# Kernel optimization log

Hardware: AMD Instinct MI355X
Metric: run time of the kernel (lower is better)

Reference implementation:

```python
import math
import jax, jax.numpy as jnp
import numpy as np

B, C_IN, C_OUT, K, STYLE_DIM, H, W = 8, 512, 512, 3, 512, 64, 64
EPS = 1e-8

def setup_inputs() -> dict:
    key = jax.random.key(0)
    k1, k2, k3, k4 = jax.random.split(key, 4)
    inp = {
        "input": jax.random.normal(k1, (B, C_IN, H, W), dtype=jnp.float32),
        "style": jax.random.normal(k2, (B, STYLE_DIM), dtype=jnp.float32),
        # learned params
        "weight": jax.random.normal(k3, (1, C_OUT, C_IN, K, K), dtype=jnp.float32),
        "mod_weight": jax.random.normal(k4, (C_IN, STYLE_DIM), dtype=jnp.float32),  # EqualLinear weight (lr_mul=1)
        "mod_bias": jnp.ones((C_IN,), dtype=jnp.float32),  # bias_init=1
    }
    return inp

def reference(input, style, weight, mod_weight, mod_bias):
    batch, in_ch, h, w = input.shape
    out_ch, ksize = weight.shape[1], weight.shape[-1]
    # EqualLinear modulation: scale = 1/sqrt(style_dim), lr_mul = 1
    mod_scale = 1.0 / math.sqrt(mod_weight.shape[1])
    s = style @ (mod_weight * mod_scale).T + mod_bias  # [B, C_in]
    # modulate weights per sample
    conv_scale = 1.0 / math.sqrt(in_ch * ksize * ksize)
    wmod = conv_scale * weight * s[:, None, :, None, None]  # [B, O, C, k, k]
    # demodulate
    demod = jax.lax.rsqrt(jnp.sum(wmod * wmod, axis=(2, 3, 4)) + EPS)  # [B, O]
    wmod = wmod * demod[:, :, None, None, None]
    # grouped conv with groups = batch
    wflat = wmod.reshape(batch * out_ch, in_ch, ksize, ksize)
    xflat = input.reshape(1, batch * in_ch, h, w)
    pad = ksize // 2
    out = jax.lax.conv_general_dilated(
        xflat, wflat,
        window_strides=(1, 1),
        padding=[(pad, pad), (pad, pad)],
        dimension_numbers=("NCHW", "OIHW", "NCHW"),
        feature_group_count=batch,
    )
    return out.reshape(batch, out_ch, h, w)
```

## Files before the change

kernel.cpp:

```cpp
#include <hip/hip_runtime.h>


typedef __bf16 bf16x8 __attribute__((ext_vector_type(8)));
typedef float f32x16 __attribute__((ext_vector_type(16)));

#define AS1 __attribute__((address_space(1)))
#define AS3 __attribute__((address_space(3)))

__device__ __forceinline__ unsigned short f2bf(float f) {
  union { float f; unsigned int u; } v; v.f = f;
  unsigned int u = v.u;
  return (unsigned short)((u + 0x7fffu + ((u >> 16) & 1u)) >> 16);
}

__global__ void k_mod(const float* __restrict__ style, const float* __restrict__ mw,
                      const float* __restrict__ mb, float* __restrict__ s,
                      float* __restrict__ zp) {
  int t = blockIdx.x * 256 + threadIdx.x;
  if (blockIdx.x == 0) {
    zp[threadIdx.x] = 0.f; zp[256 + threadIdx.x] = 0.f;
    zp[512 + threadIdx.x] = 0.f; zp[768 + threadIdx.x] = 0.f;
  }
  int b = t >> 9, c = t & 511;
  float acc = 0.f;
  for (int d = 0; d < 512; ++d) acc += style[b * 512 + d] * mw[c * 512 + d];
  s[t] = acc * 0.04419417382415922f + mb[c];
}

__global__ void k_wprep(const float* __restrict__ w, float* __restrict__ wsq,
                        unsigned short* __restrict__ wbf) {
  int t = blockIdx.x * 256 + threadIdx.x;
  int o = t >> 9, c = t & 511;
  const float* wp = w + (size_t)(o * 512 + c) * 9;
  float q = 0.f;
#pragma unroll
  for (int k = 0; k < 9; ++k) {
    float v = wp[k];
    q += v * v;
    wbf[((size_t)k * 512 + o) * 512 + c] = f2bf(v);
  }
  wsq[t] = q;
}

__global__ void k_scale(const float* __restrict__ wsq, const float* __restrict__ s,
                        float* __restrict__ scale) {
  int t = blockIdx.x * 256 + threadIdx.x;
  int b = t >> 9, o = t & 511;
  float acc = 0.f;
  for (int c = 0; c < 512; ++c) {
    float sv = s[b * 512 + c];
    acc += wsq[o * 512 + c] * sv * sv;
  }
  const float cs = 0.014731391274719739f;
  scale[t] = cs * rsqrtf(cs * cs * acc + 1e-8f);
}

__global__ void k_xt(const float* __restrict__ x, const float* __restrict__ s,
                     unsigned short* __restrict__ xt) {
  __shared__ __align__(16) unsigned short tile[64 * 65 * 8];
  int bid = blockIdx.x;
  int b = bid >> 6, y = bid & 63;
  int t = threadIdx.x;
  int co = t >> 3, xo = t & 7;
  const float* xbase = x + ((size_t)(b * 512 + co * 8) * 64 + y) * 64 + xo * 8;
  float4 v[8][2];
#pragma unroll
  for (int j = 0; j < 8; ++j) {
    v[j][0] = *(const float4*)(xbase + (size_t)j * 4096);
    v[j][1] = *(const float4*)(xbase + (size_t)j * 4096 + 4);
  }
  float sv[8];
#pragma unroll
  for (int j = 0; j < 8; ++j) sv[j] = s[b * 512 + co * 8 + j];
#pragma unroll
  for (int k = 0; k < 8; ++k) {
    unsigned short r[8];
#pragma unroll
    for (int j = 0; j < 8; ++j) {
      float f = (k < 4) ? ((const float*)&v[j][0])[k & 3]
                        : ((const float*)&v[j][1])[k & 3];
      r[j] = f2bf(f * sv[j]);
    }
    int xr = xo * 8 + k;
    int unit = xr * 65 + (co ^ xr);
    *(ulonglong2*)&tile[unit * 8] = *(ulonglong2*)r;
  }
  __syncthreads();
  unsigned short* obase = xt + ((size_t)(b * 64 + y) * 64) * 512;
#pragma unroll
  for (int i = 0; i < 8; ++i) {
    int unit_o = i * 512 + t;
    int xr = unit_o >> 6, cor = unit_o & 63;
    int unit = xr * 65 + (cor ^ xr);
    *(ulonglong2*)&obase[(size_t)unit_o * 8] = *(const ulonglong2*)&tile[unit * 8];
  }
}

#define XISS 20
#define WOFF_US 10240
#define BUFU    28672

__global__ __launch_bounds__(512, 2) void k_conv(
    const unsigned short* __restrict__ xt, const unsigned short* __restrict__ wbf,
    const float* __restrict__ scale, const float* __restrict__ zp,
    float* __restrict__ out) {
  __shared__ __align__(16) unsigned short lds[2 * BUFU];

  int bid = blockIdx.x;
  int b = bid & 7;
  int rest = bid >> 3;
  int ob = rest & 3;
  int rest2 = rest >> 2;
  int yg = rest2 & 3;
  int xg = rest2 >> 2;

  int tid = threadIdx.x;
  int wid = tid >> 6;
  int wo = wid & 1, wyy = wid >> 1;
  int lane = tid & 63, ln31 = lane & 31, hi = lane >> 5;
  int kxs = wid % 3;

  const char* srcp[7];
  const char* xglob = (const char*)(xt + (size_t)b * 64 * 64 * 512);
#pragma unroll
  for (int i = 0; i < 7; ++i) {
    int is = wid + i * 8;
    const char* p;
    if (is < XISS) {
      int e = is * 64 + lane;
      int chunk = e / 612;
      int rem = e - chunk * 612;
      int row = rem / 34;
      int xi = rem - row * 34;
      int y = yg * 16 + row - 1, x = xg * 32 + xi - 1;
      bool ok = (chunk < 2) && (y >= 0) && (y < 64) && (x >= 0) && (x < 64);
      p = ok ? xglob + 2 * ((y * 64 + x) * 512 + chunk * 8) : (const char*)zp;
    } else {
      int e2 = (is - XISS) * 64 + lane;
      int chunk = e2 / 1152;
      int rem = e2 - chunk * 1152;
      int tap = rem >> 7, o = rem & 127;
      p = (const char*)wbf + 2 * ((tap * 512 + ob * 128 + o) * 512 + chunk * 8);
    }
    srcp[i] = p;
  }

  f32x16 acc[8];
#pragma unroll
  for (int i = 0; i < 8; ++i)
    acc[i] = (f32x16){0,0,0,0,0,0,0,0,0,0,0,0,0,0,0,0};

  auto STAGE = [&](int bufu) {
#pragma unroll
    for (int i = 0; i < 7; ++i) {
      __builtin_amdgcn_global_load_lds(
          (const AS1 void*)srcp[i],
          (AS3 void*)&lds[bufu + (wid + i * 8) * 512], 16, 0, 0);
      srcp[i] += 32;
    }
  };

  auto COMPUTE = [&](const unsigned short* Xbp, const unsigned short* Abp) {
#pragma unroll
    for (int j = 0; j < 3; ++j) {
      int kx = kxs + j;
      if (kx >= 3) kx -= 3;
      const unsigned short* Xk = Xbp + kx * 8;
      const unsigned short* Ak = Abp + kx * 1024;
      bf16x8 bv[6], av[6];
#pragma unroll
      for (int rr = 0; rr < 6; ++rr)
        bv[rr] = *(const bf16x8*)&Xk[rr * 272];
#pragma unroll
      for (int ky = 0; ky < 3; ++ky) {
        av[ky * 2]     = *(const bf16x8*)&Ak[ky * 3072];
        av[ky * 2 + 1] = *(const bf16x8*)&Ak[ky * 3072 + 256];
      }
      __builtin_amdgcn_s_setprio(1);
#pragma unroll
      for (int ky = 0; ky < 3; ++ky) {
#pragma unroll
        for (int ry = 0; ry < 4; ++ry) {
          acc[ry] = __builtin_amdgcn_mfma_f32_32x32x16_bf16(
              av[ky * 2], bv[ry + ky], acc[ry], 0, 0, 0);
          acc[4 + ry] = __builtin_amdgcn_mfma_f32_32x32x16_bf16(
              av[ky * 2 + 1], bv[ry + ky], acc[4 + ry], 0, 0, 0);
        }
      }
      __builtin_amdgcn_s_setprio(0);
    }
  };

  const unsigned short* Xb0 = &lds[(hi * 612 + wyy * 4 * 34 + ln31) * 8];
  const unsigned short* Ab0 = &lds[WOFF_US + (hi * 1152 + wo * 64 + ln31) * 8];
  const unsigned short* Xb1 = Xb0 + BUFU;
  const unsigned short* Ab1 = Ab0 + BUFU;

  STAGE(0);
  asm volatile("s_waitcnt vmcnt(0) lgkmcnt(0)" ::: "memory");
  __builtin_amdgcn_s_barrier();
  __builtin_amdgcn_sched_barrier(0);

#pragma unroll 1
  for (int t = 0; t < 16; ++t) {
    STAGE(BUFU);
    COMPUTE(Xb0, Ab0);
    asm volatile("s_waitcnt vmcnt(0) lgkmcnt(0)" ::: "memory");
    __builtin_amdgcn_s_barrier();
    __builtin_amdgcn_sched_barrier(0);
    if (t < 15) STAGE(0);
    COMPUTE(Xb1, Ab1);
    asm volatile("s_waitcnt vmcnt(0) lgkmcnt(0)" ::: "memory");
    __builtin_amdgcn_s_barrier();
    __builtin_amdgcn_sched_barrier(0);
  }

  const float* scp = scale + b * 512 + ob * 128 + wo * 64;
  float* op = out + (((size_t)(b * 512 + ob * 128 + wo * 64) * 64) +
                     yg * 16 + wyy * 4) * 64 + xg * 32 + ln31;
#pragma unroll
  for (int oh = 0; oh < 2; ++oh) {
#pragma unroll
    for (int ry = 0; ry < 4; ++ry) {
      const f32x16& A = acc[oh * 4 + ry];
#pragma unroll
      for (int reg = 0; reg < 16; ++reg) {
        int orow = (reg & 3) + 8 * (reg >> 2) + hi * 4;
        int ol = oh * 32 + orow;
        op[(size_t)ol * 4096 + ry * 64] = A[reg] * scp[ol];
      }
    }
  }
}

extern "C" void kernel_launch(void* const* d_in, const int* in_sizes, int n_in,
                              void* d_out, int out_size, void* d_ws, size_t ws_size,
                              hipStream_t stream) {
  const float* x     = (const float*)d_in[0];
  const float* style = (const float*)d_in[1];
  const float* w     = (const float*)d_in[2];
  const float* mw    = (const float*)d_in[3];
  const float* mb    = (const float*)d_in[4];
  float* out = (float*)d_out;

  char* ws = (char*)d_ws;
  float* zp    = (float*)ws;
  float* s     = (float*)(ws + 4096);
  float* scale = (float*)(ws + 20480);
  float* wsq   = (float*)(ws + 36864);
  unsigned short* wbf = (unsigned short*)(ws + 1085440);
  unsigned short* xt  = (unsigned short*)(ws + 5804032);

  k_mod  <<<16,   256, 0, stream>>>(style, mw, mb, s, zp);
  k_wprep<<<1024, 256, 0, stream>>>(w, wsq, wbf);
  k_scale<<<16,   256, 0, stream>>>(wsq, s, scale);
  k_xt   <<<512,  512, 0, stream>>>(x, s, xt);
  k_conv <<<256,  512, 0, stream>>>(xt, wbf, scale, zp, out);
}
```

Before: 215.3 us.

## Halve conv waves with larger per-wave row tiles and coalesce weight prep via LDS

The conv kernel now runs 4 waves per block instead of 8. Each wave covers 8 output rows instead of 4, so it holds 16 accumulator tiles and reuses the loaded A fragments across more MFMAs. Input-fragment loads for the next kx tap are issued before the current tap's MFMAs to overlap LDS reads with compute. Weight prep now stages each output channel's weights in shared memory for coalesced reads and writes packed bf16 pairs. The cost is heavy register pressure (16 f32x16 accumulators plus doubled fragment buffers) and lower occupancy, which can cause spills or less latency hiding.

```diff
diff --git a/kernel.cpp b/kernel.cpp
--- a/kernel.cpp
+++ b/kernel.cpp
@@ -27,19 +27,28 @@
   s[t] = acc * 0.04419417382415922f + mb[c];
 }
 
-__global__ void k_wprep(const float* __restrict__ w, float* __restrict__ wsq,
-                        unsigned short* __restrict__ wbf) {
-  int t = blockIdx.x * 256 + threadIdx.x;
-  int o = t >> 9, c = t & 511;
-  const float* wp = w + (size_t)(o * 512 + c) * 9;
-  float q = 0.f;
+__global__ __launch_bounds__(256) void k_wprep(
+    const float* __restrict__ w, float* __restrict__ wsq,
+    unsigned short* __restrict__ wbf) {
+  __shared__ float wl[4608];
+  int o = blockIdx.x;
+  int t = threadIdx.x;
+  const float* wp = w + (size_t)o * 4608;
+  for (int i = t; i < 4608; i += 256) wl[i] = wp[i];
+  __syncthreads();
+  int c0 = t * 2;
+  float q0 = 0.f, q1 = 0.f;
+  unsigned int rr[9];
 #pragma unroll
   for (int k = 0; k < 9; ++k) {
-    float v = wp[k];
-    q += v * v;
-    wbf[((size_t)k * 512 + o) * 512 + c] = f2bf(v);
-  }
-  wsq[t] = q;
+    float v0 = wl[c0 * 9 + k], v1 = wl[c0 * 9 + 9 + k];
+    q0 += v0 * v0; q1 += v1 * v1;
+    rr[k] = (unsigned int)f2bf(v0) | ((unsigned int)f2bf(v1) << 16);
+  }
+  *(float2*)&wsq[o * 512 + c0] = make_float2(q0, q1);
+#pragma unroll
+  for (int k = 0; k < 9; ++k)
+    *(unsigned int*)&wbf[((size_t)k * 512 + o) * 512 + c0] = rr[k];
 }
 
 __global__ void k_scale(const float* __restrict__ wsq, const float* __restrict__ s,
@@ -100,7 +109,7 @@
 #define WOFF_US 10240
 #define BUFU    28672
 
-__global__ __launch_bounds__(512, 2) void k_conv(
+__global__ __launch_bounds__(256, 1) void k_conv(
     const unsigned short* __restrict__ xt, const unsigned short* __restrict__ wbf,
     const float* __restrict__ scale, const float* __restrict__ zp,
     float* __restrict__ out) {
@@ -118,13 +127,12 @@
   int wid = tid >> 6;
   int wo = wid & 1, wyy = wid >> 1;
   int lane = tid & 63, ln31 = lane & 31, hi = lane >> 5;
-  int kxs = wid % 3;
-
-  const char* srcp[7];
+
+  const char* srcp[14];
   const char* xglob = (const char*)(xt + (size_t)b * 64 * 64 * 512);
 #pragma unroll
-  for (int i = 0; i < 7; ++i) {
-    int is = wid + i * 8;
+  for (int i = 0; i < 14; ++i) {
+    int is = wid + i * 4;
     const char* p;
     if (is < XISS) {
       int e = is * 64 + lane;
@@ -145,53 +153,59 @@
     srcp[i] = p;
   }
 
-  f32x16 acc[8];
-#pragma unroll
-  for (int i = 0; i < 8; ++i)
+  f32x16 acc[16];
+#pragma unroll
+  for (int i = 0; i < 16; ++i)
     acc[i] = (f32x16){0,0,0,0,0,0,0,0,0,0,0,0,0,0,0,0};
 
   auto STAGE = [&](int bufu) {
 #pragma unroll
-    for (int i = 0; i < 7; ++i) {
+    for (int i = 0; i < 14; ++i) {
       __builtin_amdgcn_global_load_lds(
           (const AS1 void*)srcp[i],
-          (AS3 void*)&lds[bufu + (wid + i * 8) * 512], 16, 0, 0);
+          (AS3 void*)&lds[bufu + (wid + i * 4) * 512], 16, 0, 0);
       srcp[i] += 32;
     }
   };
 
+  auto LOADK = [&](const unsigned short* Xbp, const unsigned short* Abp,
+                   int kx, bf16x8* bv, bf16x8* av) {
+#pragma unroll
+    for (int rr = 0; rr < 10; ++rr)
+      bv[rr] = *(const bf16x8*)&Xbp[(rr * 34 + kx) * 8];
+#pragma unroll
+    for (int ky = 0; ky < 3; ++ky) {
+      av[ky * 2]     = *(const bf16x8*)&Abp[(ky * 3 + kx) * 1024];
+      av[ky * 2 + 1] = *(const bf16x8*)&Abp[(ky * 3 + kx) * 1024 + 256];
+    }
+  };
+
+  auto MFK = [&](const bf16x8* bv, const bf16x8* av) {
+    __builtin_amdgcn_s_setprio(1);
+#pragma unroll
+    for (int ky = 0; ky < 3; ++ky) {
+#pragma unroll
+      for (int ry = 0; ry < 8; ++ry) {
+        acc[ry] = __builtin_amdgcn_mfma_f32_32x32x16_bf16(
+            av[ky * 2], bv[ry + ky], acc[ry], 0, 0, 0);
+        acc[8 + ry] = __builtin_amdgcn_mfma_f32_32x32x16_bf16(
+            av[ky * 2 + 1], bv[ry + ky], acc[8 + ry], 0, 0, 0);
+      }
+    }
+    __builtin_amdgcn_s_setprio(0);
+  };
+
   auto COMPUTE = [&](const unsigned short* Xbp, const unsigned short* Abp) {
-#pragma unroll
-    for (int j = 0; j < 3; ++j) {
-      int kx = kxs + j;
-      if (kx >= 3) kx -= 3;
-      const unsigned short* Xk = Xbp + kx * 8;
-      const unsigned short* Ak = Abp + kx * 1024;
-      bf16x8 bv[6], av[6];
-#pragma unroll
-      for (int rr = 0; rr < 6; ++rr)
-        bv[rr] = *(const bf16x8*)&Xk[rr * 272];
-#pragma unroll
-      for (int ky = 0; ky < 3; ++ky) {
-        av[ky * 2]     = *(const bf16x8*)&Ak[ky * 3072];
-        av[ky * 2 + 1] = *(const bf16x8*)&Ak[ky * 3072 + 256];
-      }
-      __builtin_amdgcn_s_setprio(1);
-#pragma unroll
-      for (int ky = 0; ky < 3; ++ky) {
-#pragma unroll
-        for (int ry = 0; ry < 4; ++ry) {
-          acc[ry] = __builtin_amdgcn_mfma_f32_32x32x16_bf16(
-              av[ky * 2], bv[ry + ky], acc[ry], 0, 0, 0);
-          acc[4 + ry] = __builtin_amdgcn_mfma_f32_32x32x16_bf16(
-              av[ky * 2 + 1], bv[ry + ky], acc[4 + ry], 0, 0, 0);
-        }
-      }
-      __builtin_amdgcn_s_setprio(0);
-    }
-  };
-
-  const unsigned short* Xb0 = &lds[(hi * 612 + wyy * 4 * 34 + ln31) * 8];
+    bf16x8 b0[10], a0[6], b1[10], a1[6];
+    LOADK(Xbp, Abp, 0, b0, a0);
+    LOADK(Xbp, Abp, 1, b1, a1);
+    MFK(b0, a0);
+    LOADK(Xbp, Abp, 2, b0, a0);
+    MFK(b1, a1);
+    MFK(b0, a0);
+  };
+
+  const unsigned short* Xb0 = &lds[(hi * 612 + wyy * 272 + ln31) * 8];
   const unsigned short* Ab0 = &lds[WOFF_US + (hi * 1152 + wo * 64 + ln31) * 8];
   const unsigned short* Xb1 = Xb0 + BUFU;
   const unsigned short* Ab1 = Ab0 + BUFU;
@@ -217,12 +231,12 @@
 
   const float* scp = scale + b * 512 + ob * 128 + wo * 64;
   float* op = out + (((size_t)(b * 512 + ob * 128 + wo * 64) * 64) +
-                     yg * 16 + wyy * 4) * 64 + xg * 32 + ln31;
+                     yg * 16 + wyy * 8) * 64 + xg * 32 + ln31;
 #pragma unroll
   for (int oh = 0; oh < 2; ++oh) {
 #pragma unroll
-    for (int ry = 0; ry < 4; ++ry) {
-      const f32x16& A = acc[oh * 4 + ry];
+    for (int ry = 0; ry < 8; ++ry) {
+      const f32x16& A = acc[oh * 8 + ry];
 #pragma unroll
       for (int reg = 0; reg < 16; ++reg) {
         int orow = (reg & 3) + 8 * (reg >> 2) + hi * 4;
@@ -252,8 +266,8 @@
   unsigned short* xt  = (unsigned short*)(ws + 5804032);
 
   k_mod  <<<16,   256, 0, stream>>>(style, mw, mb, s, zp);
-  k_wprep<<<1024, 256, 0, stream>>>(w, wsq, wbf);
+  k_wprep<<<512,  256, 0, stream>>>(w, wsq, wbf);
   k_scale<<<16,   256, 0, stream>>>(wsq, s, scale);
   k_xt   <<<512,  512, 0, stream>>>(x, s, xt);
-  k_conv <<<256,  512, 0, stream>>>(xt, wbf, scale, zp, out);
-}
+  k_conv <<<256,  256, 0, stream>>>(xt, wbf, scale, zp, out);
+}
```

New measurement: 244.4 us. 13.5% more time.
